# Kernel optimization log

Measured on AMD Instinct MI355X. Metric: run time of the kernel, lower is better.

The kernel has to match this reference:

```python
import jax, jax.numpy as jnp
import numpy as np


def _apply_ring(x, angles):
    """Apply x @ R^T where R = G_0 @ G_1 @ ... @ G_{n-1} with ring planes
    (k, (k+1) % n). Equivalent to applying G_k^T to x for k = n-1 .. 0:
      x[:, k] <- c*x[:, k] - s*x[:, j]
      x[:, j] <- s*x[:, k] + c*x[:, j]
    x: [B, n], angles: [n].
    """
    n = angles.shape[0]

    def step(xT, k):
        a = angles[k]
        c, s = jnp.cos(a), jnp.sin(a)
        j = jnp.mod(k + 1, n)
        xi = xT[k]
        xj = xT[j]
        xT = xT.at[k].set(c * xi - s * xj)
        xT = xT.at[j].set(s * xi + c * xj)
        return xT, None

    ks = jnp.arange(n - 1, -1, -1)  # reverse order: R^T = G_{n-1}^T ... G_0^T
    xT, _ = jax.lax.scan(step, x.T, ks)  # carry is [n, B]
    return xT.T


def setup_inputs() -> dict:
    key = jax.random.key(0)
    k_x, k_e, k_d = jax.random.split(key, 3)
    B, n, num_blocks = 8192, 1024, 4
    return {
        "x": jax.random.normal(k_x, (B, n), dtype=jnp.float32),
        "angles_enc": jax.random.normal(k_e, (num_blocks, n), dtype=jnp.float32),
        "angles_dec": jax.random.normal(k_d, (num_blocks, n), dtype=jnp.float32),
        "hidden_weight": jnp.zeros((1,), dtype=jnp.float32),
        "hidden_state": jnp.zeros((n,), dtype=jnp.float32),
    }


def reference(x, angles_enc, angles_dec, hidden_weight, hidden_state):
    num_blocks = angles_enc.shape[0]
    b = x
    for blk in range(num_blocks):
        b = _apply_ring(b, angles_enc[blk])
    # recurrent blend; weight uses the detached hidden_weight (original uses
    # numpy on .detach()), so stop_gradient matches the original semantics.
    w = jax.nn.sigmoid(jax.lax.stop_gradient(hidden_weight[0]))
    bottleneck = (1.0 - w) * b + w * hidden_state[None, :]
    out = bottleneck
    for blk in range(num_blocks):
        out = _apply_ring(out, angles_dec[blk])
    return (bottleneck, out)
```

## Files before the change

kernel.cpp:

```cpp
#include <hip/hip_runtime.h>
#include <math.h>

#define N_COLS 1024
#define NRINGS 8

#define TPR    32
#define CHUNK  32
#define PAIRS_PER_BLOCK 8

#define F_OFF   16384
#define A_OFF   24576
#define AUX_OFF 24832
#define WS_FLOATS 24848

__global__ __launch_bounds__(256)
void ced_setup(const float* __restrict__ ae,
               const float* __restrict__ ad,
               float* __restrict__ ws)
{
    __shared__ float2 ls[256];
    const int r   = blockIdx.x >> 2;
    const int b   = blockIdx.x & 3;
    const int tid = threadIdx.x;
    const int k   = (b << 8) + tid;
    const float* ang = (r < 4) ? (ae + (r << 10)) : (ad + ((r - 4) << 10));

    float sv, cv;
    sincosf(ang[k], &sv, &cv);
    if (k == N_COLS - 1) {
        ((float2*)(ws + AUX_OFF))[r] = make_float2(cv, sv);
        cv = 0.f; sv = -1.f;
    }
    ls[tid] = make_float2(cv, sv);
    __syncthreads();

    if (!(tid & 1)) {
        float2 e0 = ls[tid], e1 = ls[tid + 1];
        int t  = k >> 5;
        int jp = (k & 31) >> 1;
        ((float4*)ws)[(r*16 + jp)*32 + t] = make_float4(e0.x, e0.y, e1.x, e1.y);
    }

    if (tid < 64) {
        const int lt = tid >> 3;
        const int q  = tid & 7;
        const int t  = (b << 3) + lt;
        const int j0 = lt * CHUNK + 4 * q;
        float2 e0 = ls[j0], e1 = ls[j0+1], e2 = ls[j0+2], e3 = ls[j0+3];

        float f3 = e3.x;       float P = -e3.y;
        float f2 = e2.x * P;   P *= -e2.y;
        float f1 = e1.x * P;   P *= -e1.y;
        float f0 = e0.x * P;   P *= -e0.y;

        float ip = P;
        #pragma unroll
        for (int d = 1; d < 8; d <<= 1) {
            float tmp = __shfl_down(ip, d);
            if (q + d < 8) ip *= tmp;
        }
        float ex = __shfl_down(ip, 1);
        if (q == 7) ex = 1.f;
        f0 *= ex; f1 *= ex; f2 *= ex; f3 *= ex;

        ((float4*)(ws + F_OFF))[(r*8 + q)*32 + t] = make_float4(f0, f1, f2, f3);
        if (q == 0) ws[A_OFF + r*TPR + t] = ip;
    }
}

__global__ __launch_bounds__(256, 2)
void ced_main(const float* __restrict__ x,
              const float* __restrict__ ws,
              const float* __restrict__ hw,
              const float* __restrict__ hs,
              float* __restrict__ out, int B)
{
    const float4* CS  = (const float4*)ws;
    const float4* F   = (const float4*)(ws + F_OFF);
    const float*  A   = ws + A_OFF;
    const float2* AUX = (const float2*)(ws + AUX_OFF);

    const int tid  = threadIdx.x;
    const int lane = tid & 63;
    const int t    = lane & 31;
    const int groupBase = lane & 32;
    const int pair = blockIdx.x * PAIRS_PER_BLOCK + (tid >> 5);

    const size_t rowA = (size_t)(2 * pair) * N_COLS;
    const size_t rowB = rowA + N_COLS;

    float ya[CHUNK], yb[CHUNK];
    {
        const float4* xa = (const float4*)(x + rowA + t * CHUNK);
        const float4* xb = (const float4*)(x + rowB + t * CHUNK);
        #pragma unroll
        for (int i = 0; i < 8; ++i) {
            float4 va = xa[i], vb = xb[i];
            ya[4*i] = va.x; ya[4*i+1] = va.y; ya[4*i+2] = va.z; ya[4*i+3] = va.w;
            yb[4*i] = vb.x; yb[4*i+1] = vb.y; yb[4*i+2] = vb.z; yb[4*i+3] = vb.w;
        }
    }

    const float w   = 1.f / (1.f + expf(-hw[0]));
    const float omw = 1.f - w;

    #pragma unroll 1
    for (int r = 0; r < NRINGS; ++r) {
        if (r == 4) {
            float4* oa = (float4*)(out + rowA + t * CHUNK);
            float4* ob = (float4*)(out + rowB + t * CHUNK);
            const float4* hp = (const float4*)(hs + t * CHUNK);
            #pragma unroll
            for (int i = 0; i < 8; ++i) {
                float4 h = hp[i];
                float4 na, nb;
                na.x = fmaf(omw, ya[4*i+0], w * h.x);
                na.y = fmaf(omw, ya[4*i+1], w * h.y);
                na.z = fmaf(omw, ya[4*i+2], w * h.z);
                na.w = fmaf(omw, ya[4*i+3], w * h.w);
                nb.x = fmaf(omw, yb[4*i+0], w * h.x);
                nb.y = fmaf(omw, yb[4*i+1], w * h.y);
                nb.z = fmaf(omw, yb[4*i+2], w * h.z);
                nb.w = fmaf(omw, yb[4*i+3], w * h.w);
                oa[i] = na; ob[i] = nb;
                ya[4*i+0] = na.x; ya[4*i+1] = na.y; ya[4*i+2] = na.z; ya[4*i+3] = na.w;
                yb[4*i+0] = nb.x; yb[4*i+1] = nb.y; yb[4*i+2] = nb.z; yb[4*i+3] = nb.w;
            }
        }

        const float4* csr = CS + r * 512 + t;
        float4 cs_all[16];
        #pragma unroll
        for (int jp = 0; jp < 16; ++jp) cs_all[jp] = csr[jp * 32];

        const float2 cN = AUX[r];
        float y0a = __shfl(ya[0],       groupBase);
        float yNa = __shfl(ya[CHUNK-1], groupBase + 31);
        float y0b = __shfl(yb[0],       groupBase);
        float yNb = __shfl(yb[CHUNK-1], groupBase + 31);
        float CinitA = cN.x * yNa - cN.y * y0a;
        float CinitB = cN.x * yNb - cN.y * y0b;
        float x0nA   = fmaf(cN.y, yNa, cN.x * y0a);
        float x0nB   = fmaf(cN.y, yNb, cN.x * y0b);
        if (t == 0) { ya[0] = x0nA; yb[0] = x0nB; }

        float carA = 0.f, carB = 0.f, ztA = 0.f, ztB = 0.f;
        #pragma unroll
        for (int jp = CHUNK/2 - 1; jp >= 0; --jp) {
            float4 cs4 = cs_all[jp];
            const int j1 = 2*jp + 1;
            float z1a = fmaf(cs4.w, ya[j1], cs4.z * carA);
            float z1b = fmaf(cs4.w, yb[j1], cs4.z * carB);
            carA = fmaf(-cs4.w, carA, cs4.z * ya[j1]);
            carB = fmaf(-cs4.w, carB, cs4.z * yb[j1]);
            if (j1 == CHUNK - 1) { ztA = z1a; ztB = z1b; }
            else                 { ya[j1+1] = z1a; yb[j1+1] = z1b; }
            const int j0 = 2*jp;
            float z0a = fmaf(cs4.y, ya[j0], cs4.x * carA);
            float z0b = fmaf(cs4.y, yb[j0], cs4.x * carB);
            carA = fmaf(-cs4.y, carA, cs4.x * ya[j0]);
            carB = fmaf(-cs4.y, carB, cs4.x * yb[j0]);
            ya[j0+1] = z0a; yb[j0+1] = z0b;
        }

        const float4* fr = F + r * 256 + t;
        float4 f_all[8];
        #pragma unroll
        for (int qi = 0; qi < 8; ++qi) f_all[qi] = fr[qi * 32];

        float sa = A[r*32 + t];
        float sbA = carA, sbB = carB;
        #pragma unroll
        for (int d = 1; d < TPR; d <<= 1) {
            float a2  = __shfl_down(sa,  d);
            float b2a = __shfl_down(sbA, d);
            float b2b = __shfl_down(sbB, d);
            if (t + d < TPR) {
                sbA = fmaf(sa, b2a, sbA);
                sbB = fmaf(sa, b2b, sbB);
                sa *= a2;
            }
        }
        float ea  = __shfl_down(sa,  1);
        float ebA = __shfl_down(sbA, 1);
        float ebB = __shfl_down(sbB, 1);
        float zfA = fmaf(sa, CinitA, sbA);
        float zfB = fmaf(sa, CinitB, sbB);
        float CinA = (t == TPR - 1) ? CinitA : fmaf(ea, CinitA, ebA);
        float CinB = (t == TPR - 1) ? CinitB : fmaf(ea, CinitB, ebB);

        #pragma unroll
        for (int qi = CHUNK/4 - 1; qi >= 0; --qi) {
            float4 f4 = f_all[qi];
            const int j = 4*qi;
            if (j + 3 == CHUNK - 1) { ztA = fmaf(f4.w, CinA, ztA);
                                      ztB = fmaf(f4.w, CinB, ztB); }
            else                    { ya[j+4] = fmaf(f4.w, CinA, ya[j+4]);
                                      yb[j+4] = fmaf(f4.w, CinB, yb[j+4]); }
            ya[j+3] = fmaf(f4.z, CinA, ya[j+3]);  yb[j+3] = fmaf(f4.z, CinB, yb[j+3]);
            ya[j+2] = fmaf(f4.y, CinA, ya[j+2]);  yb[j+2] = fmaf(f4.y, CinB, yb[j+2]);
            ya[j+1] = fmaf(f4.x, CinA, ya[j+1]);  yb[j+1] = fmaf(f4.x, CinB, yb[j+1]);
        }

        float upA = __shfl_up(ztA, 1);
        float upB = __shfl_up(ztB, 1);
        ya[0] = (t == 0) ? zfA : upA;
        yb[0] = (t == 0) ? zfB : upB;
    }

    float4* oa = (float4*)(out + (size_t)B * N_COLS + rowA + t * CHUNK);
    float4* ob = (float4*)(out + (size_t)B * N_COLS + rowB + t * CHUNK);
    #pragma unroll
    for (int i = 0; i < 8; ++i) {
        oa[i] = make_float4(ya[4*i], ya[4*i+1], ya[4*i+2], ya[4*i+3]);
        ob[i] = make_float4(yb[4*i], yb[4*i+1], yb[4*i+2], yb[4*i+3]);
    }
}

__global__ __launch_bounds__(256, 2)
void ced_fallback(const float* __restrict__ x,
                  const float* __restrict__ ae,
                  const float* __restrict__ ad,
                  const float* __restrict__ hw,
                  const float* __restrict__ hs,
                  float* __restrict__ out, int B)
{
    __shared__ float2 s_cs[NRINGS * 64 * 16];
    __shared__ float  s_A [NRINGS * 16];
    __shared__ float2 s_aux[NRINGS];

    const int tid = threadIdx.x;
    for (int i = 0; i < 32; ++i) {
        int idx = i * 256 + tid;
        int r   = idx >> 10;
        int k   = idx & 1023;
        const float* ang = (r < 4) ? (ae + (r << 10)) : (ad + ((r - 4) << 10));
        float sv, cv;
        sincosf(ang[k], &sv, &cv);
        int t = k >> 6, j = k & 63;
        float2 e = make_float2(cv, sv);
        if (k == 1023) { s_aux[r] = e; e = make_float2(0.f, -1.f); }
        s_cs[(r * 64 + j) * 16 + t] = e;
    }
    __syncthreads();
    if (tid < NRINGS * 16) {
        int r = tid >> 4, t = tid & 15;
        float p = 1.f;
        for (int j = 0; j < 64; ++j) p *= -s_cs[(r * 64 + j) * 16 + t].y;
        s_A[tid] = p;
    }
    __syncthreads();

    const int lane      = tid & 63;
    const int g         = lane >> 4;
    const int t         = lane & 15;
    const int groupBase = lane & 48;
    const int row       = blockIdx.x * 16 + (tid >> 6) * 4 + g;

    const float* xr = x + (size_t)row * N_COLS + t * 64;
    float y[64];
    #pragma unroll
    for (int i = 0; i < 16; ++i) {
        float4 v = ((const float4*)xr)[i];
        y[4*i] = v.x; y[4*i+1] = v.y; y[4*i+2] = v.z; y[4*i+3] = v.w;
    }
    const float w   = 1.f / (1.f + expf(-hw[0]));
    const float omw = 1.f - w;

    for (int r = 0; r < NRINGS; ++r) {
        if (r == 4) {
            float4* ob = (float4*)(out + (size_t)row * N_COLS + t * 64);
            const float4* hp = (const float4*)(hs + t * 64);
            #pragma unroll
            for (int i = 0; i < 16; ++i) {
                float4 h = hp[i];
                float4 bn;
                bn.x = fmaf(omw, y[4*i+0], w * h.x);
                bn.y = fmaf(omw, y[4*i+1], w * h.y);
                bn.z = fmaf(omw, y[4*i+2], w * h.z);
                bn.w = fmaf(omw, y[4*i+3], w * h.w);
                ob[i] = bn;
                y[4*i+0] = bn.x; y[4*i+1] = bn.y; y[4*i+2] = bn.z; y[4*i+3] = bn.w;
            }
        }
        const float2* csr = s_cs + r * 64 * 16;
        const float2  cN  = s_aux[r];
        float y0 = __shfl(y[0],  groupBase);
        float yN = __shfl(y[63], groupBase + 15);
        float Cinit = cN.x * yN - cN.y * y0;
        float x0n   = fmaf(cN.y, yN, cN.x * y0);
        if (t == 0) y[0] = x0n;

        float carry = 0.f, ztmp = 0.f;
        #pragma unroll
        for (int j = 63; j >= 0; --j) {
            float2 cs = csr[j * 16 + t];
            float z   = fmaf(cs.y, y[j], cs.x * carry);
            carry     = fmaf(-cs.y, carry, cs.x * y[j]);
            if (j == 63) ztmp = z; else y[j + 1] = z;
        }
        float sa = s_A[r * 16 + t], sb = carry;
        #pragma unroll
        for (int d = 1; d < 16; d <<= 1) {
            float a2 = __shfl_down(sa, d);
            float b2 = __shfl_down(sb, d);
            if (t + d < 16) { sb = fmaf(sa, b2, sb); sa *= a2; }
        }
        float ea = __shfl_down(sa, 1);
        float eb = __shfl_down(sb, 1);
        float z0  = fmaf(sa, Cinit, sb);
        float Cin = (t == 15) ? Cinit : fmaf(ea, Cinit, eb);

        float P = 1.f;
        #pragma unroll
        for (int j = 63; j >= 0; --j) {
            float2 cs = csr[j * 16 + t];
            float f = cs.x * P;
            P = -cs.y * P;
            if (j == 63) ztmp = fmaf(f, Cin, ztmp);
            else         y[j + 1] = fmaf(f, Cin, y[j + 1]);
        }
        float up = __shfl_up(ztmp, 1);
        y[0] = (t == 0) ? z0 : up;
    }

    float4* oo = (float4*)(out + (size_t)B * N_COLS + (size_t)row * N_COLS + t * 64);
    #pragma unroll
    for (int i = 0; i < 16; ++i)
        oo[i] = make_float4(y[4*i], y[4*i+1], y[4*i+2], y[4*i+3]);
}

extern "C" void kernel_launch(void* const* d_in, const int* in_sizes, int n_in,
                              void* d_out, int out_size, void* d_ws, size_t ws_size,
                              hipStream_t stream) {
    const float* x  = (const float*)d_in[0];
    const float* ae = (const float*)d_in[1];
    const float* ad = (const float*)d_in[2];
    const float* hw = (const float*)d_in[3];
    const float* hs = (const float*)d_in[4];
    float* out = (float*)d_out;
    const int B = in_sizes[0] / N_COLS;

    if (ws_size >= WS_FLOATS * sizeof(float)) {
        hipLaunchKernelGGL(ced_setup, dim3(32), dim3(256), 0, stream,
                           ae, ad, (float*)d_ws);
        hipLaunchKernelGGL(ced_main, dim3(B / (2 * PAIRS_PER_BLOCK)), dim3(256), 0, stream,
                           x, (const float*)d_ws, hw, hs, out, B);
    } else {
        hipLaunchKernelGGL(ced_fallback, dim3(B / 16), dim3(256), 0, stream,
                           x, ae, ad, hw, hs, out, B);
    }
}
```

Before: 136.7 us.

## Stage ring coefficients in double-buffered LDS via async global-to-LDS loads

The main kernel now copies the per-ring cos/sin and correction-factor tables into shared memory, two rings per phase. It uses __builtin_amdgcn_global_load_lds into a double buffer, so the next pair of rings is prefetched while the current pair is computed. The inner loops read coefficients from LDS as they need them, instead of loading 16+8 float4 per thread from global memory into registers before each ring. This is meant to hide global-load latency and free registers. In exchange it costs about 49KB of LDS per block and adds block-wide barriers between phases.

```diff
diff --git a/kernel.cpp b/kernel.cpp
--- a/kernel.cpp
+++ b/kernel.cpp
@@ -12,6 +12,9 @@
 #define A_OFF   24576
 #define AUX_OFF 24832
 #define WS_FLOATS 24848
+
+typedef const __attribute__((address_space(1))) float4* gas_f4;
+typedef __attribute__((address_space(3))) void* las_ptr;
 
 __global__ __launch_bounds__(256)
 void ced_setup(const float* __restrict__ ae,
@@ -75,19 +78,33 @@
               const float* __restrict__ hs,
               float* __restrict__ out, int B)
 {
-    const float4* CS  = (const float4*)ws;
-    const float4* F   = (const float4*)(ws + F_OFF);
-    const float*  A   = ws + A_OFF;
-    const float2* AUX = (const float2*)(ws + AUX_OFF);
+    __shared__ float4 sCS[2][1024];
+    __shared__ float4 sF [2][512];
+    __shared__ float4 sA4[64];
+    __shared__ float4 sAux4[4];
+
+    const float4* CSg = (const float4*)ws;
+    const float4* Fg  = (const float4*)(ws + F_OFF);
 
     const int tid  = threadIdx.x;
     const int lane = tid & 63;
     const int t    = lane & 31;
     const int groupBase = lane & 32;
-    const int pair = blockIdx.x * PAIRS_PER_BLOCK + (tid >> 5);
-
-    const size_t rowA = (size_t)(2 * pair) * N_COLS;
+    const int pairRow = blockIdx.x * PAIRS_PER_BLOCK + (tid >> 5);
+    const size_t rowA = (size_t)(2 * pairRow) * N_COLS;
     const size_t rowB = rowA + N_COLS;
+
+    #pragma unroll
+    for (int m = 0; m < 4; ++m)
+        __builtin_amdgcn_global_load_lds((gas_f4)(CSg + m*256 + tid),
+                                         (las_ptr)&sCS[0][m*256 + tid], 16, 0, 0);
+    #pragma unroll
+    for (int m = 0; m < 2; ++m)
+        __builtin_amdgcn_global_load_lds((gas_f4)(Fg + m*256 + tid),
+                                         (las_ptr)&sF[0][m*256 + tid], 16, 0, 0);
+
+    if (tid < 64)              sA4[tid]        = ((const float4*)(ws + A_OFF))[tid];
+    if (tid >= 64 && tid < 68) sAux4[tid - 64] = ((const float4*)(ws + AUX_OFF))[tid - 64];
 
     float ya[CHUNK], yb[CHUNK];
     {
@@ -104,108 +121,129 @@
     const float w   = 1.f / (1.f + expf(-hw[0]));
     const float omw = 1.f - w;
 
+    __syncthreads();
+
+    const float*  As   = (const float*)sA4;
+    const float2* Auxs = (const float2*)sAux4;
+
     #pragma unroll 1
-    for (int r = 0; r < NRINGS; ++r) {
-        if (r == 4) {
-            float4* oa = (float4*)(out + rowA + t * CHUNK);
-            float4* ob = (float4*)(out + rowB + t * CHUNK);
-            const float4* hp = (const float4*)(hs + t * CHUNK);
-            #pragma unroll
-            for (int i = 0; i < 8; ++i) {
-                float4 h = hp[i];
-                float4 na, nb;
-                na.x = fmaf(omw, ya[4*i+0], w * h.x);
-                na.y = fmaf(omw, ya[4*i+1], w * h.y);
-                na.z = fmaf(omw, ya[4*i+2], w * h.z);
-                na.w = fmaf(omw, ya[4*i+3], w * h.w);
-                nb.x = fmaf(omw, yb[4*i+0], w * h.x);
-                nb.y = fmaf(omw, yb[4*i+1], w * h.y);
-                nb.z = fmaf(omw, yb[4*i+2], w * h.z);
-                nb.w = fmaf(omw, yb[4*i+3], w * h.w);
-                oa[i] = na; ob[i] = nb;
-                ya[4*i+0] = na.x; ya[4*i+1] = na.y; ya[4*i+2] = na.z; ya[4*i+3] = na.w;
-                yb[4*i+0] = nb.x; yb[4*i+1] = nb.y; yb[4*i+2] = nb.z; yb[4*i+3] = nb.w;
-            }
-        }
-
-        const float4* csr = CS + r * 512 + t;
-        float4 cs_all[16];
-        #pragma unroll
-        for (int jp = 0; jp < 16; ++jp) cs_all[jp] = csr[jp * 32];
-
-        const float2 cN = AUX[r];
-        float y0a = __shfl(ya[0],       groupBase);
-        float yNa = __shfl(ya[CHUNK-1], groupBase + 31);
-        float y0b = __shfl(yb[0],       groupBase);
-        float yNb = __shfl(yb[CHUNK-1], groupBase + 31);
-        float CinitA = cN.x * yNa - cN.y * y0a;
-        float CinitB = cN.x * yNb - cN.y * y0b;
-        float x0nA   = fmaf(cN.y, yNa, cN.x * y0a);
-        float x0nB   = fmaf(cN.y, yNb, cN.x * y0b);
-        if (t == 0) { ya[0] = x0nA; yb[0] = x0nB; }
-
-        float carA = 0.f, carB = 0.f, ztA = 0.f, ztB = 0.f;
-        #pragma unroll
-        for (int jp = CHUNK/2 - 1; jp >= 0; --jp) {
-            float4 cs4 = cs_all[jp];
-            const int j1 = 2*jp + 1;
-            float z1a = fmaf(cs4.w, ya[j1], cs4.z * carA);
-            float z1b = fmaf(cs4.w, yb[j1], cs4.z * carB);
-            carA = fmaf(-cs4.w, carA, cs4.z * ya[j1]);
-            carB = fmaf(-cs4.w, carB, cs4.z * yb[j1]);
-            if (j1 == CHUNK - 1) { ztA = z1a; ztB = z1b; }
-            else                 { ya[j1+1] = z1a; yb[j1+1] = z1b; }
-            const int j0 = 2*jp;
-            float z0a = fmaf(cs4.y, ya[j0], cs4.x * carA);
-            float z0b = fmaf(cs4.y, yb[j0], cs4.x * carB);
-            carA = fmaf(-cs4.y, carA, cs4.x * ya[j0]);
-            carB = fmaf(-cs4.y, carB, cs4.x * yb[j0]);
-            ya[j0+1] = z0a; yb[j0+1] = z0b;
-        }
-
-        const float4* fr = F + r * 256 + t;
-        float4 f_all[8];
-        #pragma unroll
-        for (int qi = 0; qi < 8; ++qi) f_all[qi] = fr[qi * 32];
-
-        float sa = A[r*32 + t];
-        float sbA = carA, sbB = carB;
-        #pragma unroll
-        for (int d = 1; d < TPR; d <<= 1) {
-            float a2  = __shfl_down(sa,  d);
-            float b2a = __shfl_down(sbA, d);
-            float b2b = __shfl_down(sbB, d);
-            if (t + d < TPR) {
-                sbA = fmaf(sa, b2a, sbA);
-                sbB = fmaf(sa, b2b, sbB);
-                sa *= a2;
-            }
-        }
-        float ea  = __shfl_down(sa,  1);
-        float ebA = __shfl_down(sbA, 1);
-        float ebB = __shfl_down(sbB, 1);
-        float zfA = fmaf(sa, CinitA, sbA);
-        float zfB = fmaf(sa, CinitB, sbB);
-        float CinA = (t == TPR - 1) ? CinitA : fmaf(ea, CinitA, ebA);
-        float CinB = (t == TPR - 1) ? CinitB : fmaf(ea, CinitB, ebB);
-
-        #pragma unroll
-        for (int qi = CHUNK/4 - 1; qi >= 0; --qi) {
-            float4 f4 = f_all[qi];
-            const int j = 4*qi;
-            if (j + 3 == CHUNK - 1) { ztA = fmaf(f4.w, CinA, ztA);
-                                      ztB = fmaf(f4.w, CinB, ztB); }
-            else                    { ya[j+4] = fmaf(f4.w, CinA, ya[j+4]);
-                                      yb[j+4] = fmaf(f4.w, CinB, yb[j+4]); }
-            ya[j+3] = fmaf(f4.z, CinA, ya[j+3]);  yb[j+3] = fmaf(f4.z, CinB, yb[j+3]);
-            ya[j+2] = fmaf(f4.y, CinA, ya[j+2]);  yb[j+2] = fmaf(f4.y, CinB, yb[j+2]);
-            ya[j+1] = fmaf(f4.x, CinA, ya[j+1]);  yb[j+1] = fmaf(f4.x, CinB, yb[j+1]);
-        }
-
-        float upA = __shfl_up(ztA, 1);
-        float upB = __shfl_up(ztB, 1);
-        ya[0] = (t == 0) ? zfA : upA;
-        yb[0] = (t == 0) ? zfB : upB;
+    for (int p = 0; p < 4; ++p) {
+        if (p < 3) {
+            const int nb = (p + 1) & 1;
+            const float4* gc = CSg + (p + 1) * 1024;
+            const float4* gf = Fg  + (p + 1) * 512;
+            #pragma unroll
+            for (int m = 0; m < 4; ++m)
+                __builtin_amdgcn_global_load_lds((gas_f4)(gc + m*256 + tid),
+                                                 (las_ptr)&sCS[nb][m*256 + tid], 16, 0, 0);
+            #pragma unroll
+            for (int m = 0; m < 2; ++m)
+                __builtin_amdgcn_global_load_lds((gas_f4)(gf + m*256 + tid),
+                                                 (las_ptr)&sF[nb][m*256 + tid], 16, 0, 0);
+        }
+
+        const int buf = p & 1;
+        #pragma unroll
+        for (int lr = 0; lr < 2; ++lr) {
+            const int rr = 2 * p + lr;
+
+            if (p == 2 && lr == 0) {
+                float4* oa = (float4*)(out + rowA + t * CHUNK);
+                float4* ob = (float4*)(out + rowB + t * CHUNK);
+                const float4* hp = (const float4*)(hs + t * CHUNK);
+                #pragma unroll
+                for (int i = 0; i < 8; ++i) {
+                    float4 h = hp[i];
+                    float4 na, nb2;
+                    na.x  = fmaf(omw, ya[4*i+0], w * h.x);
+                    na.y  = fmaf(omw, ya[4*i+1], w * h.y);
+                    na.z  = fmaf(omw, ya[4*i+2], w * h.z);
+                    na.w  = fmaf(omw, ya[4*i+3], w * h.w);
+                    nb2.x = fmaf(omw, yb[4*i+0], w * h.x);
+                    nb2.y = fmaf(omw, yb[4*i+1], w * h.y);
+                    nb2.z = fmaf(omw, yb[4*i+2], w * h.z);
+                    nb2.w = fmaf(omw, yb[4*i+3], w * h.w);
+                    oa[i] = na; ob[i] = nb2;
+                    ya[4*i+0] = na.x;  ya[4*i+1] = na.y;  ya[4*i+2] = na.z;  ya[4*i+3] = na.w;
+                    yb[4*i+0] = nb2.x; yb[4*i+1] = nb2.y; yb[4*i+2] = nb2.z; yb[4*i+3] = nb2.w;
+                }
+            }
+
+            const float4* csL = &sCS[buf][lr * 512];
+            const float4* fL  = &sF [buf][lr * 256];
+            const float2  cN  = Auxs[rr];
+            const float   saI = As[rr * TPR + t];
+
+            float y0a = __shfl(ya[0],       groupBase);
+            float yNa = __shfl(ya[CHUNK-1], groupBase + 31);
+            float y0b = __shfl(yb[0],       groupBase);
+            float yNb = __shfl(yb[CHUNK-1], groupBase + 31);
+            float CinitA = cN.x * yNa - cN.y * y0a;
+            float CinitB = cN.x * yNb - cN.y * y0b;
+            float x0nA   = fmaf(cN.y, yNa, cN.x * y0a);
+            float x0nB   = fmaf(cN.y, yNb, cN.x * y0b);
+            if (t == 0) { ya[0] = x0nA; yb[0] = x0nB; }
+
+            float carA = 0.f, carB = 0.f, ztA = 0.f, ztB = 0.f;
+            #pragma unroll
+            for (int jp = CHUNK/2 - 1; jp >= 0; --jp) {
+                float4 cs4 = csL[jp * 32 + t];
+                const int j1 = 2*jp + 1;
+                float z1a = fmaf(cs4.w, ya[j1], cs4.z * carA);
+                float z1b = fmaf(cs4.w, yb[j1], cs4.z * carB);
+                carA = fmaf(-cs4.w, carA, cs4.z * ya[j1]);
+                carB = fmaf(-cs4.w, carB, cs4.z * yb[j1]);
+                if (j1 == CHUNK - 1) { ztA = z1a; ztB = z1b; }
+                else                 { ya[j1+1] = z1a; yb[j1+1] = z1b; }
+                const int j0 = 2*jp;
+                float z0a = fmaf(cs4.y, ya[j0], cs4.x * carA);
+                float z0b = fmaf(cs4.y, yb[j0], cs4.x * carB);
+                carA = fmaf(-cs4.y, carA, cs4.x * ya[j0]);
+                carB = fmaf(-cs4.y, carB, cs4.x * yb[j0]);
+                ya[j0+1] = z0a; yb[j0+1] = z0b;
+            }
+
+            float sa = saI;
+            float sbA = carA, sbB = carB;
+            #pragma unroll
+            for (int d = 1; d < TPR; d <<= 1) {
+                float a2  = __shfl_down(sa,  d);
+                float b2a = __shfl_down(sbA, d);
+                float b2b = __shfl_down(sbB, d);
+                if (t + d < TPR) {
+                    sbA = fmaf(sa, b2a, sbA);
+                    sbB = fmaf(sa, b2b, sbB);
+                    sa *= a2;
+                }
+            }
+            float ea  = __shfl_down(sa,  1);
+            float ebA = __shfl_down(sbA, 1);
+            float ebB = __shfl_down(sbB, 1);
+            float zfA = fmaf(sa, CinitA, sbA);
+            float zfB = fmaf(sa, CinitB, sbB);
+            float CinA = (t == TPR - 1) ? CinitA : fmaf(ea, CinitA, ebA);
+            float CinB = (t == TPR - 1) ? CinitB : fmaf(ea, CinitB, ebB);
+
+            #pragma unroll
+            for (int qi = CHUNK/4 - 1; qi >= 0; --qi) {
+                float4 f4 = fL[qi * 32 + t];
+                const int j = 4*qi;
+                if (j + 3 == CHUNK - 1) { ztA = fmaf(f4.w, CinA, ztA);
+                                          ztB = fmaf(f4.w, CinB, ztB); }
+                else                    { ya[j+4] = fmaf(f4.w, CinA, ya[j+4]);
+                                          yb[j+4] = fmaf(f4.w, CinB, yb[j+4]); }
+                ya[j+3] = fmaf(f4.z, CinA, ya[j+3]);  yb[j+3] = fmaf(f4.z, CinB, yb[j+3]);
+                ya[j+2] = fmaf(f4.y, CinA, ya[j+2]);  yb[j+2] = fmaf(f4.y, CinB, yb[j+2]);
+                ya[j+1] = fmaf(f4.x, CinA, ya[j+1]);  yb[j+1] = fmaf(f4.x, CinB, yb[j+1]);
+            }
+
+            float upA = __shfl_up(ztA, 1);
+            float upB = __shfl_up(ztB, 1);
+            ya[0] = (t == 0) ? zfA : upA;
+            yb[0] = (t == 0) ? zfB : upB;
+        }
+
+        if (p < 3) __syncthreads();
     }
 
     float4* oa = (float4*)(out + (size_t)B * N_COLS + rowA + t * CHUNK);
```

New measurement: 124.6 us. 1.1x faster.
